# Performance work log

Measured on AMD Instinct MI355X. Metric: run time of the kernel, lower is better.

Reference implementation:

```python
import jax, jax.numpy as jnp
import numpy as np

K, PS, WS, WT, NHEADS, STRIDE0_A, STRIDE0 = 7, 7, 8, 1, 1, 8, 4
SCALE = STRIDE0_A // STRIDE0  # index-upsampling factor (coarse stride 8 -> fine stride 4)


def _reflect(i, L):
    # dnls-style reflect bounds: i<0 -> -i, i>=L -> 2*(L-1)-i (single reflection suffices here)
    i = jnp.abs(i)
    return jnp.where(i >= L, 2 * (L - 1) - i, i)


def _patch_offsets(ps):
    pr = jnp.arange(ps) - ps // 2
    return jnp.stack(jnp.meshgrid(pr, pr, indexing='ij'), -1).reshape(-1, 2)  # [ps*ps, 2]


def _exact_search(vid0, vid1):
    # coarse windowed patch-product k-NN search (prod_with_heads), stride0_a query grid
    B, T, C, H, W = vid0.shape
    HD, Ch = NHEADS, C // NHEADS
    v0 = jnp.moveaxis(vid0, 2, -1)  # [B,T,H,W,C]
    v1 = jnp.moveaxis(vid1, 2, -1)
    nH, nW = H // STRIDE0_A, W // STRIDE0_A
    qt, qi, qj = [a.reshape(-1) for a in jnp.meshgrid(jnp.arange(T), jnp.arange(nH), jnp.arange(nW), indexing='ij')]
    qh, qw = qi * STRIDE0_A, qj * STRIDE0_A
    Q = qt.shape[0]
    st = 2 * WT + 1  # temporal window, shifted to stay in [0,T)
    t0 = jnp.clip(qt - WT, 0, T - st)
    offs = jnp.arange(WS) - WS // 2  # spatial window offsets, stride1=1
    ct = jnp.broadcast_to((t0[:, None] + jnp.arange(st))[:, :, None, None], (Q, st, WS, WS)).reshape(Q, -1)
    ch = jnp.broadcast_to((qh[:, None] + offs)[:, None, :, None], (Q, st, WS, WS)).reshape(Q, -1)
    cw = jnp.broadcast_to((qw[:, None] + offs)[:, None, None, :], (Q, st, WS, WS)).reshape(Q, -1)
    S = st * WS * WS
    poffs = _patch_offsets(PS)

    def body(acc, off):  # accumulate patch inner products one patch-pixel at a time (memory-light)
        dr, dc = off[0], off[1]
        p0 = v0[:, qt, _reflect(qh + dr, H), _reflect(qw + dc, W)]   # [B,Q,C]
        p1 = v1[:, ct, _reflect(ch + dr, H), _reflect(cw + dc, W)]   # [B,Q,S,C]
        d = jnp.einsum('bqnc,bqsnc->bnqs', p0.reshape(B, Q, HD, Ch), p1.reshape(B, Q, S, HD, Ch))
        return acc + d, None

    dists, _ = jax.lax.scan(jax.checkpoint(body), jnp.zeros((B, HD, Q, S), v0.dtype), poffs)
    vals, idx = jax.lax.top_k(dists, K)  # product search -> largest first
    qsel = jnp.arange(Q)[None, None, :, None]
    inds = jnp.stack([ct[qsel, idx], ch[qsel, idx], cw[qsel, idx]], -1)  # [B,HD,Q,K,3]
    return vals, inds


def _upsample_inds(inds_a, T, H, W):
    # interpolate_inds: replicate coarse inds to the fine stride0 grid, shifted by the
    # fine-query offset relative to its parent coarse query; anchor self at slot 0.
    nH, nW = H // STRIDE0_A, W // STRIDE0_A
    nHf, nWf = H // STRIDE0, W // STRIDE0
    ft, fi, fj = [a.reshape(-1) for a in jnp.meshgrid(jnp.arange(T), jnp.arange(nHf), jnp.arange(nWf), indexing='ij')]
    fh, fw = fi * STRIDE0, fj * STRIDE0
    ci = jnp.clip(fi // SCALE, 0, nH - 1)
    cj = jnp.clip(fj // SCALE, 0, nW - 1)
    qlin = ft * nH * nW + ci * nW + cj
    base = inds_a[:, :, qlin]  # [B,HD,Qf,K,3]
    dh = (fh - ci * STRIDE0_A)[None, None, :, None]
    dw = (fw - cj * STRIDE0_A)[None, None, :, None]
    it = base[..., 0]
    ih = _reflect(base[..., 1] + dh, H)
    iw = _reflect(base[..., 2] + dw, W)
    it = it.at[..., 0].set(ft[None, None, :])  # anchor_self=True
    ih = ih.at[..., 0].set(fh[None, None, :])
    iw = iw.at[..., 0].set(fw[None, None, :])
    return (ft, fh, fw), (it, ih, iw)


def _refine_dists(vid0, vid1, fq, cand):
    # prod_refine with ws_r=1: evaluate the patch product exactly at the given inds
    B, T, C, H, W = vid0.shape
    HD, Ch = NHEADS, C // NHEADS
    ft, fh, fw = fq
    it, ih, iw = cand
    Qf, k = it.shape[2], it.shape[3]
    v0 = jnp.moveaxis(vid0, 2, -1)                                # [B,T,H,W,C]
    v1h = jnp.moveaxis(vid1, 2, -1).reshape(B, T, H, W, HD, Ch)
    bidx = jnp.arange(B)[:, None, None, None]
    hidx = jnp.arange(HD)[None, :, None, None]
    poffs = _patch_offsets(PS)

    def body(acc, off):
        dr, dc = off[0], off[1]
        p0 = v0[:, ft, _reflect(fh + dr, H), _reflect(fw + dc, W)]              # [B,Qf,C]
        p1 = v1h[bidx, it, _reflect(ih + dr, H), _reflect(iw + dc, W), hidx]    # [B,HD,Qf,k,Ch]
        d = jnp.einsum('bqnc,bnqkc->bnqk', p0.reshape(B, Qf, HD, Ch), p1)
        return acc + d, None

    dists, _ = jax.lax.scan(jax.checkpoint(body), jnp.zeros((B, HD, Qf, k), v0.dtype), poffs)
    return dists


def setup_inputs() -> dict:
    key = jax.random.key(0)
    k0, k1 = jax.random.split(key)
    B, T, C, H, W = 1, 3, 64, 192, 192
    vid0 = jax.random.normal(k0, (B, T, C, H, W), dtype=jnp.float32)
    vid1 = jax.random.normal(k1, (B, T, C, H, W), dtype=jnp.float32)
    flows = jnp.zeros((B, T, 2, H, W), dtype=jnp.float32)  # accepted but unused (fflow/bflow=None)
    return {"vid0": vid0, "vid1": vid1, "flows": flows}


def reference(vid0, vid1, flows):
    B, T, C, H, W = vid0.shape
    dists_a, inds_a = _exact_search(vid0, vid1)            # coarse stride0_a search
    fq, cand = _upsample_inds(inds_a, T, H, W)             # interpolate inds to stride0 grid
    dists_f = _refine_dists(vid0, vid1, fq, cand)          # refine (fill) dists at fine inds
    inds_f = jnp.stack(cand, -1)                           # [B,HD,Qf,K,3]
    return dists_f, inds_f
```

## Files before the change

kernel.cpp:

```cpp
#include <hip/hip_runtime.h>
#include <math.h>

#define TT   3
#define CC   64
#define HH   192
#define WW   192
#define HWW  (HH*WW)
#define NHC  24
#define NWC  24
#define QC   1728
#define SC   192
#define NPIX 49
#define KK   7
#define NHF  48
#define NWF  48
#define QF   6912

__device__ __forceinline__ int reflect(int i, int L) {
  i = i < 0 ? -i : i;
  return (i >= L) ? (2 * (L - 1) - i) : i;
}

__global__ void transpose_tchw_thwc(const float* __restrict__ in0,
                                    const float* __restrict__ in1,
                                    float* __restrict__ out0,
                                    float* __restrict__ out1) {
  const float* in = blockIdx.y ? in1 : in0;
  float* out = blockIdx.y ? out1 : out0;
  int b = blockIdx.x;
  int x0 = (b % 3) * 64;
  int ty = b / 3;
  int t = ty / HH, y = ty % HH;

  __shared__ float tile[64][65];
  int lx = threadIdx.x & 63;
  int lc = threadIdx.x >> 6;

  const float* src = in + (size_t)t * CC * HWW + (size_t)y * WW + x0;
#pragma unroll
  for (int i = 0; i < 16; ++i) {
    int c = lc + i * 4;
    tile[c][lx] = src[(size_t)c * HWW + lx];
  }
  __syncthreads();
  float* dst = out + ((size_t)(t * HH + y) * WW + x0) * CC;
#pragma unroll
  for (int i = 0; i < 16; ++i) {
    int x = lc + i * 4;
    dst[(size_t)x * CC + lx] = tile[lx][x];
  }
}

__global__ __launch_bounds__(256, 4) void coarse_fma_kernel(
    const float* __restrict__ v0, const float* __restrict__ v1,
    float* __restrict__ dists) {
  int bid = blockIdx.x;
  int q = (bid & 7) * (QC / 8) + (bid >> 3);
  int qt = q / (NHC * NWC);
  int r = q % (NHC * NWC);
  int qh = (r / NWC) * 8;
  int qw = (r % NWC) * 8;

  __shared__ float4 region4[8 * 196];
  __shared__ float4 qbuf4[16 * 49];
  float* wbuf = (float*)region4;

  int tid = threadIdx.x;
  int s = tid & 63;
  int w = tid >> 6;
  int oi = s >> 3, oj = s & 7;

  int pxb[13];
#pragma unroll
  for (int i = 0; i < 13; ++i) {
    int p = w + 4 * i;
    if (p > 48) p = 48;
    pxb[i] = ((oi + p / 7) * 14 + (oj + p % 7)) * 16;
  }

  {
    const float* b0 = v0 + (size_t)qt * HWW * CC;
    for (int idx = tid; idx < 896; idx += 256) {
      int p = (idx & 7) | ((idx >> 7) << 3);
      int c4 = (idx >> 3) & 15;
      if (p < 49) {
        int ry = reflect(qh + p / 7 - 3, HH);
        int rx = reflect(qw + p % 7 - 3, WW);
        qbuf4[c4 * 49 + p] = *reinterpret_cast<const float4*>(
            b0 + ((size_t)ry * WW + rx) * CC + c4 * 4);
      }
    }
  }

  for (int ct = 0; ct < 3; ++ct) {
    const float* b1 = v1 + (size_t)ct * HWW * CC;
    float acc[13];
#pragma unroll
    for (int i = 0; i < 13; ++i) acc[i] = 0.f;

#pragma unroll
    for (int h = 0; h < 2; ++h) {
      __syncthreads();
      for (int idx = tid; idx < 1600; idx += 256) {
        int px = (idx & 7) | ((idx >> 6) << 3);
        int c4h = (idx >> 3) & 7;
        if (px < 196) {
          int ry = reflect(qh - 7 + px / 14, HH);
          int rx = reflect(qw - 7 + px % 14, WW);
          region4[c4h * 196 + px] = *reinterpret_cast<const float4*>(
              b1 + ((size_t)ry * WW + rx) * CC + (h * 8 + c4h) * 4);
        }
      }
      __syncthreads();

#pragma unroll
      for (int i = 0; i < 13; ++i) {
        if (i < 12 || w == 0) {
          int p = w + 4 * i;
          const char* rbase = reinterpret_cast<const char*>(region4) + pxb[i];
#pragma unroll
          for (int c4h = 0; c4h < 8; ++c4h) {
            float4 a = qbuf4[(h * 8 + c4h) * 49 + p];
            float4 b = *reinterpret_cast<const float4*>(rbase + c4h * 3136);
            acc[i] = fmaf(a.x, b.x, acc[i]);
            acc[i] = fmaf(a.y, b.y, acc[i]);
            acc[i] = fmaf(a.z, b.z, acc[i]);
            acc[i] = fmaf(a.w, b.w, acc[i]);
          }
        }
      }
    }

    __syncthreads();
#pragma unroll
    for (int i = 0; i < 13; ++i) {
      if (i < 12 || w == 0) wbuf[s * 49 + (w + 4 * i)] = acc[i];
    }
    __syncthreads();
    if (tid < 64) {
      float a = 0.f;
      const float* wr = wbuf + tid * 49;
      for (int p = 0; p < NPIX; ++p)
        a = __fadd_rn(a, wr[p]);
      dists[(size_t)q * SC + ct * 64 + tid] = a;
    }
  }
}

__global__ __launch_bounds__(256) void topk_kernel(
    const float* __restrict__ dists, int* __restrict__ topk) {
  int q = blockIdx.x * 4 + (threadIdx.x >> 6);
  if (q >= QC) return;
  int lane = threadIdx.x & 63;
  const float* d = dists + (size_t)q * SC;
  float v[3] = {d[lane], d[lane + 64], d[lane + 128]};
  int tk = 0;
#pragma unroll
  for (int k = 0; k < KK; ++k) {
    float bv = -INFINITY;
    int bi = 0x7fffffff;
#pragma unroll
    for (int j = 0; j < 3; ++j) {
      if (!((tk >> j) & 1) && v[j] > bv) { bv = v[j]; bi = lane + j * 64; }
    }
#pragma unroll
    for (int off = 32; off > 0; off >>= 1) {
      float ov = __shfl_xor(bv, off, 64);
      int oi = __shfl_xor(bi, off, 64);
      if (ov > bv || (ov == bv && oi < bi)) { bv = ov; bi = oi; }
    }
    if ((bi & 63) == lane) tk |= 1 << (bi >> 6);
    if (lane == 0) topk[q * KK + k] = bi;
  }
}

__global__ __launch_bounds__(448, 7) void refine_kernel(
    const float* __restrict__ v0, const float* __restrict__ v1,
    const int* __restrict__ topk, float* __restrict__ out) {
  int bid = blockIdx.x;
  int f = (bid & 7) * (QF / 8) + (bid >> 3);
  int ft = f / (NHF * NWF);
  int r = f % (NHF * NWF);
  int fi = r / NWF, fj = r % NWF;
  int fh = fi * 4, fw = fj * 4;
  int ci = fi >> 1, cj = fj >> 1;
  int dh = (fi & 1) * 4, dw = (fj & 1) * 4;
  int qlin = ft * (NHC * NWC) + ci * NWC + cj;

  int tid = threadIdx.x;
  int lane = tid & 63;
  int k = tid >> 6;

  __shared__ float qs[NPIX * CC];

  {
    const float* b0 = v0 + (size_t)ft * HWW * CC;
#pragma unroll
    for (int i = 0; i < 7; ++i) {
      int idx = tid + i * 448;
      int p = idx >> 6, c = idx & 63;
      int ry = reflect(fh + p / 7 - 3, HH);
      int rx = reflect(fw + p % 7 - 3, WW);
      qs[idx] = b0[((size_t)ry * WW + rx) * CC + c];
    }
  }
  __syncthreads();

  int it, ih, iw;
  if (k == 0) {
    it = ft; ih = fh; iw = fw;
  } else {
    int s = topk[qlin * KK + k];
    int ti = s >> 6;
    int oi = (s >> 3) & 7, oj = s & 7;
    it = ti;
    ih = reflect(ci * 8 + oi - 4 + dh, HH);
    iw = reflect(cj * 8 + oj - 4 + dw, WW);
  }

  const float* b1 = v1 + (size_t)it * HWW * CC;
  float acc = 0.f;
#pragma unroll
  for (int pr = 0; pr < 7; ++pr) {
    int ry = reflect(ih + pr - 3, HH);
    const float* rowp = b1 + (size_t)ry * WW * CC + lane;
    float vals[7];
#pragma unroll
    for (int pc = 0; pc < 7; ++pc) {
      int rx = reflect(iw + pc - 3, WW);
      vals[pc] = rowp[(size_t)rx * CC];
    }
#pragma unroll
    for (int pc = 0; pc < 7; ++pc)
      acc = fmaf(qs[(pr * 7 + pc) * CC + lane], vals[pc], acc);
  }
#pragma unroll
  for (int off = 32; off > 0; off >>= 1)
    acc += __shfl_xor(acc, off, 64);
  if (lane == 0) {
    float* dout = out;
    float* iout = out + (size_t)QF * KK;
    dout[(size_t)f * KK + k] = acc;
    float* ip = iout + ((size_t)f * KK + k) * 3;
    ip[0] = (float)it;
    ip[1] = (float)ih;
    ip[2] = (float)iw;
  }
}

extern "C" void kernel_launch(void* const* d_in, const int* in_sizes, int n_in,
                              void* d_out, int out_size, void* d_ws,
                              size_t ws_size, hipStream_t stream) {
  const float* vid0 = (const float*)d_in[0];
  const float* vid1 = (const float*)d_in[1];
  float* out = (float*)d_out;

  char* ws = (char*)d_ws;
  float* dists = (float*)ws;
  size_t off = (size_t)QC * SC * sizeof(float);
  int* topk = (int*)(ws + off);
  off += (size_t)QC * KK * sizeof(int);
  off = (off + 255) & ~(size_t)255;
  float* v0t = (float*)(ws + off);
  size_t vbytes = (size_t)TT * HWW * CC * sizeof(float);
  float* v1t = (float*)(ws + off + vbytes);

  transpose_tchw_thwc<<<dim3(TT * HH * (WW / 64), 2), 256, 0, stream>>>(
      vid0, vid1, v0t, v1t);
  coarse_fma_kernel<<<QC, 256, 0, stream>>>(v0t, v1t, dists);
  topk_kernel<<<(QC * 64 + 255) / 256, 256, 0, stream>>>(dists, topk);
  refine_kernel<<<QF, 448, 0, stream>>>(v0t, v1t, topk, out);
}
```

Baseline: 275.1 us.

## Fuse top-k into coarse search kernel and shrink region tile for occupancy

The separate top-k kernel is folded into the coarse search kernel, with the 192 distances per query kept in shared memory instead of a global scratch buffer. The search region's channel chunk is halved (4 float4s per pass, 4 passes instead of 2), which cuts shared memory per block, and launch bounds rise to 6 blocks per CU. This saves a kernel launch and the global dists round-trip, and should raise occupancy, at the cost of twice as many barrier-separated load phases.

```diff
diff --git a/kernel.cpp b/kernel.cpp
--- a/kernel.cpp
+++ b/kernel.cpp
@@ -51,9 +51,9 @@
   }
 }
 
-__global__ __launch_bounds__(256, 4) void coarse_fma_kernel(
+__global__ __launch_bounds__(256, 6) void coarse_fma_kernel(
     const float* __restrict__ v0, const float* __restrict__ v1,
-    float* __restrict__ dists) {
+    int* __restrict__ topk) {
   int bid = blockIdx.x;
   int q = (bid & 7) * (QC / 8) + (bid >> 3);
   int qt = q / (NHC * NWC);
@@ -61,8 +61,9 @@
   int qh = (r / NWC) * 8;
   int qw = (r % NWC) * 8;
 
-  __shared__ float4 region4[8 * 196];
+  __shared__ float4 region4[4 * 196];
   __shared__ float4 qbuf4[16 * 49];
+  __shared__ float  dall[SC];
   float* wbuf = (float*)region4;
 
   int tid = threadIdx.x;
@@ -99,16 +100,16 @@
     for (int i = 0; i < 13; ++i) acc[i] = 0.f;
 
 #pragma unroll
-    for (int h = 0; h < 2; ++h) {
+    for (int ph = 0; ph < 4; ++ph) {
       __syncthreads();
-      for (int idx = tid; idx < 1600; idx += 256) {
-        int px = (idx & 7) | ((idx >> 6) << 3);
-        int c4h = (idx >> 3) & 7;
+      for (int idx = tid; idx < 1024; idx += 256) {
+        int px = (idx & 7) | ((idx >> 5) << 3);
+        int c4h = (idx >> 3) & 3;
         if (px < 196) {
           int ry = reflect(qh - 7 + px / 14, HH);
           int rx = reflect(qw - 7 + px % 14, WW);
           region4[c4h * 196 + px] = *reinterpret_cast<const float4*>(
-              b1 + ((size_t)ry * WW + rx) * CC + (h * 8 + c4h) * 4);
+              b1 + ((size_t)ry * WW + rx) * CC + (ph * 4 + c4h) * 4);
         }
       }
       __syncthreads();
@@ -119,8 +120,8 @@
           int p = w + 4 * i;
           const char* rbase = reinterpret_cast<const char*>(region4) + pxb[i];
 #pragma unroll
-          for (int c4h = 0; c4h < 8; ++c4h) {
-            float4 a = qbuf4[(h * 8 + c4h) * 49 + p];
+          for (int c4h = 0; c4h < 4; ++c4h) {
+            float4 a = qbuf4[(ph * 4 + c4h) * 49 + p];
             float4 b = *reinterpret_cast<const float4*>(rbase + c4h * 3136);
             acc[i] = fmaf(a.x, b.x, acc[i]);
             acc[i] = fmaf(a.y, b.y, acc[i]);
@@ -142,35 +143,32 @@
       const float* wr = wbuf + tid * 49;
       for (int p = 0; p < NPIX; ++p)
         a = __fadd_rn(a, wr[p]);
-      dists[(size_t)q * SC + ct * 64 + tid] = a;
-    }
-  }
-}
-
-__global__ __launch_bounds__(256) void topk_kernel(
-    const float* __restrict__ dists, int* __restrict__ topk) {
-  int q = blockIdx.x * 4 + (threadIdx.x >> 6);
-  if (q >= QC) return;
-  int lane = threadIdx.x & 63;
-  const float* d = dists + (size_t)q * SC;
-  float v[3] = {d[lane], d[lane + 64], d[lane + 128]};
-  int tk = 0;
-#pragma unroll
-  for (int k = 0; k < KK; ++k) {
-    float bv = -INFINITY;
-    int bi = 0x7fffffff;
-#pragma unroll
-    for (int j = 0; j < 3; ++j) {
-      if (!((tk >> j) & 1) && v[j] > bv) { bv = v[j]; bi = lane + j * 64; }
-    }
-#pragma unroll
-    for (int off = 32; off > 0; off >>= 1) {
-      float ov = __shfl_xor(bv, off, 64);
-      int oi = __shfl_xor(bi, off, 64);
-      if (ov > bv || (ov == bv && oi < bi)) { bv = ov; bi = oi; }
-    }
-    if ((bi & 63) == lane) tk |= 1 << (bi >> 6);
-    if (lane == 0) topk[q * KK + k] = bi;
+      dall[ct * 64 + tid] = a;
+    }
+  }
+
+  __syncthreads();
+  if (tid < 64) {
+    int lane = tid;
+    float v[3] = {dall[lane], dall[lane + 64], dall[lane + 128]};
+    int tk = 0;
+#pragma unroll
+    for (int k = 0; k < KK; ++k) {
+      float bv = -INFINITY;
+      int bi = 0x7fffffff;
+#pragma unroll
+      for (int j = 0; j < 3; ++j) {
+        if (!((tk >> j) & 1) && v[j] > bv) { bv = v[j]; bi = lane + j * 64; }
+      }
+#pragma unroll
+      for (int off = 32; off > 0; off >>= 1) {
+        float ov = __shfl_xor(bv, off, 64);
+        int oi2 = __shfl_xor(bi, off, 64);
+        if (ov > bv || (ov == bv && oi2 < bi)) { bv = ov; bi = oi2; }
+      }
+      if ((bi & 63) == lane) tk |= 1 << (bi >> 6);
+      if (lane == 0) topk[q * KK + k] = bi;
+    }
   }
 }
 
@@ -256,10 +254,8 @@
   float* out = (float*)d_out;
 
   char* ws = (char*)d_ws;
-  float* dists = (float*)ws;
-  size_t off = (size_t)QC * SC * sizeof(float);
-  int* topk = (int*)(ws + off);
-  off += (size_t)QC * KK * sizeof(int);
+  int* topk = (int*)ws;
+  size_t off = (size_t)QC * KK * sizeof(int);
   off = (off + 255) & ~(size_t)255;
   float* v0t = (float*)(ws + off);
   size_t vbytes = (size_t)TT * HWW * CC * sizeof(float);
@@ -267,7 +263,6 @@
 
   transpose_tchw_thwc<<<dim3(TT * HH * (WW / 64), 2), 256, 0, stream>>>(
       vid0, vid1, v0t, v1t);
-  coarse_fma_kernel<<<QC, 256, 0, stream>>>(v0t, v1t, dists);
-  topk_kernel<<<(QC * 64 + 255) / 256, 256, 0, stream>>>(dists, topk);
+  coarse_fma_kernel<<<QC, 256, 0, stream>>>(v0t, v1t, topk);
   refine_kernel<<<QF, 448, 0, stream>>>(v0t, v1t, topk, out);
 }
```

After: 278.8 us. No clear change (+1.3%).
